# Performance work log

Hardware: AMD Instinct MI355X
Metric: run time of the kernel (lower is better)

Reference implementation:

```python
import jax, jax.numpy as jnp
import numpy as np

N = 12288          # atoms
G = 12             # graphs in batch
R = 1536           # residues
K = 32             # max_num_neighbors
RADIUS = 5.0
MIN_DISTANCE = 5
EPS = 1e-10


def setup_inputs() -> dict:
    key = jax.random.key(0)
    k1, k2, k3 = jax.random.split(key, 3)
    # positions in a 50 A box -> protein-like density (~a few neighbors in r=5)
    node_position = jax.random.uniform(k1, (N, 3), dtype=jnp.float32) * 50.0
    node2graph = jnp.sort(jax.random.randint(k2, (N,), 0, G, dtype=jnp.int32))
    atom2residue = jnp.sort(jax.random.randint(k3, (N,), 0, R, dtype=jnp.int32))
    return {"node_position": node_position, "node2graph": node2graph,
            "atom2residue": atom2residue}


def _select_neighbors(node_position, node2graph):
    """For each node i, pick up to K nearest same-graph nodes within RADIUS.
    Returns idx [N,K] (neighbor indices) and in_radius [N,K] (validity)."""
    n = node_position.shape[0]
    sq = jnp.sum(node_position * node_position, axis=-1)            # [N]
    d2 = sq[:, None] + sq[None, :] - 2.0 * (node_position @ node_position.T)
    d2 = jnp.maximum(d2, 0.0)                                        # [N,N]
    ar = jnp.arange(n)
    valid = (node2graph[:, None] == node2graph[None, :]) \
            & (ar[:, None] != ar[None, :]) \
            & (d2 <= RADIUS * RADIUS)
    nd2 = jnp.where(valid, d2, jnp.inf)
    neg_d2, idx = jax.lax.top_k(-nd2, K)                             # nearest K
    in_radius = jnp.isfinite(neg_d2)
    return idx, in_radius


def reference(node_position, node2graph, atom2residue):
    n = node_position.shape[0]
    idx, in_radius = _select_neighbors(node_position, node2graph)
    node_out = jnp.repeat(jnp.arange(n, dtype=jnp.int32), K)         # center i
    node_in = idx.reshape(-1).astype(jnp.int32)                      # neighbor j
    valid = in_radius.reshape(-1)
    # residue-distance filter: drop |res_in - res_out| < min_distance
    res_diff = jnp.abs(atom2residue[node_in] - atom2residue[node_out])
    valid = valid & (res_diff >= MIN_DISTANCE)
    # drop near-coincident positions (||p_i - p_j|| < eps)
    diff = node_position[node_in] - node_position[node_out]
    d2_sel = jnp.sum(diff * diff, axis=-1)
    valid = valid & (d2_sel >= EPS * EPS)
    relation = jnp.zeros_like(node_in)
    edge_list = jnp.stack([node_in, node_out, relation], axis=-1)    # [N*K,3]
    edge_list = jnp.where(valid[:, None], edge_list, -1)             # pad invalid
    return edge_list, valid, jnp.int32(1)
```

## Files before the change

### kernel.cpp

```cpp
#include <hip/hip_runtime.h>

#define EDGE_K 32
#define CAP    128
#define NB     64
#define DEPTH  8

__device__ __forceinline__ int prefix_count(unsigned long long mask) {
    return (int)__builtin_amdgcn_mbcnt_hi((unsigned)(mask >> 32),
                __builtin_amdgcn_mbcnt_lo((unsigned)mask, 0u));
}

__global__ __launch_bounds__(256) void pack_kernel(
    const float* __restrict__ pos, const int* __restrict__ n2g,
    float4* __restrict__ pk, int* __restrict__ bounds, int n)
{
    int i = blockIdx.x * blockDim.x + threadIdx.x;
    if (i >= n) return;
    pk[i] = make_float4(pos[3*i+0], pos[3*i+1], pos[3*i+2], 0.0f);
    const int gi = n2g[i];
    if (i == 0) {
        for (int g = 0; g <= gi && g < NB; ++g) bounds[g] = 0;
    } else {
        const int gp = n2g[i-1];
        if (gp != gi) for (int g = gp + 1; g <= gi && g < NB; ++g) bounds[g] = i;
    }
    if (i == n - 1) {
        for (int g = gi + 1; g < NB; ++g) bounds[g] = n;
    }
}

__global__ __launch_bounds__(64) void spatial_edge_fast(
    const float4* __restrict__ pk,
    const int* __restrict__ n2g,
    const int* __restrict__ a2r,
    const int* __restrict__ bounds,
    int* __restrict__ out, int n)
{
    const int i    = blockIdx.x;
    const int lane = threadIdx.x;

    __shared__ int2 scand[CAP];
    __shared__ int2 sres[EDGE_K];
    __shared__ int2 ebuf2[EDGE_K * 3 / 2];

    const float4 pi = pk[i];
    const float xi = pi.x, yi = pi.y, zi = pi.z;
    const float si = xi*xi + yi*yi + zi*zi;
    const int g  = n2g[i];
    const int ri = a2r[i];

    int jstart, jend;
    if (g < NB - 1) {
        jstart = bounds[g];
        jend   = bounds[g + 1];
    } else {
        int lo = 0, hi = n;
        while (lo < hi) { int m = (lo + hi) >> 1; if (n2g[m] < g) lo = m + 1; else hi = m; }
        jstart = lo; hi = n;
        while (lo < hi) { int m = (lo + hi) >> 1; if (n2g[m] <= g) lo = m + 1; else hi = m; }
        jend = lo;
    }

    int count = 0;
    auto process = [&](float4 p, int j) {
        bool pass = false; float d2 = 0.0f;
        if (j < jend && j != i) {
            const float sj2 = p.x*p.x + p.y*p.y + p.z*p.z;
            const float dt  = xi*p.x + yi*p.y + zi*p.z;
            d2 = si + sj2 - 2.0f*dt;
            d2 = fmaxf(d2, 0.0f);
            pass = (d2 <= 25.0f);
        }
        const unsigned long long mask = __ballot(pass);
        if (pass) {
            const int idx = count + prefix_count(mask);
            if (idx < CAP) scand[idx] = make_int2(__float_as_int(d2), j);
        }
        count += __popcll(mask);
    };

    const int nch  = (jend - jstart + 63) >> 6;
    const int jm   = jend - 1;
    const int base = jstart + lane;

    float4 buf[DEPTH];
#pragma unroll
    for (int u = 0; u < DEPTH; ++u)
        buf[u] = pk[min(base + (u << 6), jm)];

    for (int c = 0; c < nch; c += DEPTH) {
        float4 nxt[DEPTH];
        const int nb = base + ((c + DEPTH) << 6);
#pragma unroll
        for (int u = 0; u < DEPTH; ++u)
            nxt[u] = pk[min(nb + (u << 6), jm)];
        const int ja = jstart + (c << 6) + lane;
#pragma unroll
        for (int u = 0; u < DEPTH; ++u) {
            if (c + u < nch) process(buf[u], ja + (u << 6));
        }
#pragma unroll
        for (int u = 0; u < DEPTH; ++u) buf[u] = nxt[u];
    }
    __syncthreads();

    int cnt = 0;
    if (count <= CAP) {
        const int m = count;
        for (int c = lane; c < m; c += 64) {
            const int2 e = scand[c];
            const float dc = __int_as_float(e.x);
            int rank = 0;
            for (int t = 0; t < m; ++t) {
                const int2 et = scand[t];
                const float dtv = __int_as_float(et.x);
                rank += (dtv < dc) || (dtv == dc && et.y < e.y);
            }
            if (rank < EDGE_K) sres[rank] = e;
        }
        cnt = (m < EDGE_K) ? m : EDGE_K;
    } else {
        if (lane == 0) {
            float bd[EDGE_K]; int bj[EDGE_K]; int c2 = 0;
            for (int j = jstart; j < jend; ++j) {
                if (j == i) continue;
                const float4 p = pk[j];
                const float sj2 = p.x*p.x + p.y*p.y + p.z*p.z;
                const float dt  = xi*p.x + yi*p.y + zi*p.z;
                float d2 = si + sj2 - 2.0f*dt;
                d2 = fmaxf(d2, 0.0f);
                if (d2 > 25.0f) continue;
                if (c2 == EDGE_K && d2 >= bd[EDGE_K-1]) continue;
                int p2 = (c2 < EDGE_K) ? c2 : (EDGE_K - 1);
                while (p2 > 0 && bd[p2-1] > d2) { bd[p2] = bd[p2-1]; bj[p2] = bj[p2-1]; --p2; }
                bd[p2] = d2; bj[p2] = j;
                if (c2 < EDGE_K) ++c2;
            }
            for (int k = 0; k < c2; ++k) sres[k] = make_int2(__float_as_int(bd[k]), bj[k]);
        }
        cnt = (count < EDGE_K) ? count : EDGE_K;
    }
    __syncthreads();

    const int NK = n * EDGE_K;
    int* valid_out = out + 3 * NK;
    int* eb = (int*)ebuf2;
    if (lane < EDGE_K) {
        const int k = lane;
        int a = -1, b = -1, c = -1, v = 0;
        if (k < cnt) {
            const int j = sres[k].y;
            const int rj = a2r[j];
            const int rd = (rj > ri) ? (rj - ri) : (ri - rj);
            const float4 p = pk[j];
            const float dx = p.x - xi, dy = p.y - yi, dz = p.z - zi;
            const float d2s = dx*dx + dy*dy + dz*dz;
            if (rd >= 5 && d2s >= 1e-20f) { a = j; b = i; c = 0; v = 1; }
        }
        eb[3*k+0] = a;
        eb[3*k+1] = b;
        eb[3*k+2] = c;
        valid_out[i * EDGE_K + k] = v;
    }
    __syncthreads();
    if (lane < 48) {
        int2* eo = (int2*)(out + 3 * (i * EDGE_K));
        eo[lane] = ebuf2[lane];
    }
    if (i == 0 && lane == 0) out[4*NK] = 1;
}

__global__ __launch_bounds__(64) void spatial_edge_ref(
    const float* __restrict__ pos,
    const int* __restrict__ n2g,
    const int* __restrict__ a2r,
    int* __restrict__ out, int n)
{
    const int i = blockIdx.x;
    const int lane = threadIdx.x;
    __shared__ float sd2[CAP]; __shared__ int sj[CAP];
    __shared__ float rd2[EDGE_K]; __shared__ int rjj[EDGE_K];

    const float xi = pos[3*i+0], yi = pos[3*i+1], zi = pos[3*i+2];
    const float si = xi*xi + yi*yi + zi*zi;
    const int g = n2g[i]; const int ri = a2r[i];

    int lo = 0, hi = n;
    while (lo < hi) { int m = (lo + hi) >> 1; if (n2g[m] < g) lo = m + 1; else hi = m; }
    const int jstart = lo; hi = n;
    while (lo < hi) { int m = (lo + hi) >> 1; if (n2g[m] <= g) lo = m + 1; else hi = m; }
    const int jend = lo;

    int count = 0;
    for (int j0 = jstart; j0 < jend; j0 += 64) {
        const int j = j0 + lane;
        bool pass = false; float d2 = 0.0f;
        if (j < jend && j != i) {
            const float xj = pos[3*j+0], yj = pos[3*j+1], zj = pos[3*j+2];
            const float sj2 = xj*xj + yj*yj + zj*zj;
            const float dt  = xi*xj + yi*yj + zi*zj;
            d2 = fmaxf(si + sj2 - 2.0f*dt, 0.0f);
            pass = (d2 <= 25.0f);
        }
        const unsigned long long mask = __ballot(pass);
        if (pass) {
            const int idx = count + prefix_count(mask);
            if (idx < CAP) { sd2[idx] = d2; sj[idx] = j; }
        }
        count += __popcll(mask);
    }
    __syncthreads();

    int cnt;
    if (count <= CAP) {
        const int m = count;
        for (int c = lane; c < m; c += 64) {
            const float dc = sd2[c]; const int jc = sj[c];
            int rank = 0;
            for (int t = 0; t < m; ++t)
                rank += (sd2[t] < dc) || (sd2[t] == dc && sj[t] < jc);
            if (rank < EDGE_K) { rd2[rank] = dc; rjj[rank] = jc; }
        }
        cnt = (m < EDGE_K) ? m : EDGE_K;
    } else {
        if (lane == 0) {
            float bd[EDGE_K]; int bj[EDGE_K]; int c2 = 0;
            for (int j = jstart; j < jend; ++j) {
                if (j == i) continue;
                const float xj = pos[3*j+0], yj = pos[3*j+1], zj = pos[3*j+2];
                const float sj2 = xj*xj + yj*yj + zj*zj;
                const float dt  = xi*xj + yi*yj + zi*zj;
                float d2 = fmaxf(si + sj2 - 2.0f*dt, 0.0f);
                if (d2 > 25.0f) continue;
                if (c2 == EDGE_K && d2 >= bd[EDGE_K-1]) continue;
                int p = (c2 < EDGE_K) ? c2 : (EDGE_K - 1);
                while (p > 0 && bd[p-1] > d2) { bd[p] = bd[p-1]; bj[p] = bj[p-1]; --p; }
                bd[p] = d2; bj[p] = j;
                if (c2 < EDGE_K) ++c2;
            }
            for (int k = 0; k < c2; ++k) { rd2[k] = bd[k]; rjj[k] = bj[k]; }
        }
        cnt = (count < EDGE_K) ? count : EDGE_K;
    }
    __syncthreads();

    const int NK = n * EDGE_K;
    int* valid_out = out + 3 * NK;
    if (lane < EDGE_K) {
        const int k = lane;
        int a = -1, b = -1, c = -1, v = 0;
        if (k < cnt) {
            const int j = rjj[k];
            const int rj = a2r[j];
            const int rd = (rj > ri) ? (rj - ri) : (ri - rj);
            const float dx = pos[3*j+0] - xi, dy = pos[3*j+1] - yi, dz = pos[3*j+2] - zi;
            const float d2s = dx*dx + dy*dy + dz*dz;
            if (rd >= 5 && d2s >= 1e-20f) { a = j; b = i; c = 0; v = 1; }
        }
        const int e = i * EDGE_K + k;
        out[3*e+0] = a; out[3*e+1] = b; out[3*e+2] = c;
        valid_out[e] = v;
    }
    if (i == 0 && lane == 0) out[4*NK] = 1;
}

extern "C" void kernel_launch(void* const* d_in, const int* in_sizes, int n_in,
                              void* d_out, int out_size, void* d_ws, size_t ws_size,
                              hipStream_t stream) {
    const float* pos = (const float*)d_in[0];
    const int*   n2g = (const int*)d_in[1];
    const int*   a2r = (const int*)d_in[2];
    int* out = (int*)d_out;
    const int n = in_sizes[0] / 3;
    const size_t need = (size_t)n * sizeof(float4) + NB * sizeof(int);
    const bool packed = (ws_size >= need) && (((uintptr_t)d_ws & 15) == 0);
    if (packed) {
        float4* pk = (float4*)d_ws;
        int* bounds = (int*)(pk + n);
        hipLaunchKernelGGL(pack_kernel, dim3((n + 255) / 256), dim3(256), 0, stream,
                           pos, n2g, pk, bounds, n);
        hipLaunchKernelGGL(spatial_edge_fast, dim3(n), dim3(64), 0, stream,
                           (const float4*)pk, n2g, a2r, (const int*)bounds, out, n);
    } else {
        hipLaunchKernelGGL(spatial_edge_ref, dim3(n), dim3(64), 0, stream,
                           pos, n2g, a2r, out, n);
    }
}
```

Before: 29.23 us.

## Pack four independent wavefronts per block with per-wave shared buffers

Each block now runs four wavefronts, each handling its own atom with private slices of shared memory, so the grid shrinks fourfold. The block-wide barriers become block-scope memory fences on the assumption that one wave's lanes stay in lockstep. The goal is to cut per-block launch and scheduling overhead and raise occupancy for many tiny 64-thread blocks. It relies on intra-wave LDS ordering without a real barrier, which is fragile; an early return for out-of-range waves is safe only because no block barrier remains.

```diff
diff --git a/kernel.cpp b/kernel.cpp
--- a/kernel.cpp
+++ b/kernel.cpp
@@ -4,6 +4,7 @@
 #define CAP    128
 #define NB     64
 #define DEPTH  8
+#define WPB    4
 
 __device__ __forceinline__ int prefix_count(unsigned long long mask) {
     return (int)__builtin_amdgcn_mbcnt_hi((unsigned)(mask >> 32),
@@ -29,19 +30,21 @@
     }
 }
 
-__global__ __launch_bounds__(64) void spatial_edge_fast(
+__global__ __launch_bounds__(WPB * 64) void spatial_edge_fast(
     const float4* __restrict__ pk,
     const int* __restrict__ n2g,
     const int* __restrict__ a2r,
     const int* __restrict__ bounds,
     int* __restrict__ out, int n)
 {
-    const int i    = blockIdx.x;
-    const int lane = threadIdx.x;
-
-    __shared__ int2 scand[CAP];
-    __shared__ int2 sres[EDGE_K];
-    __shared__ int2 ebuf2[EDGE_K * 3 / 2];
+    const int wave = threadIdx.x >> 6;
+    const int lane = threadIdx.x & 63;
+    const int i    = blockIdx.x * WPB + wave;
+    if (i >= n) return;
+
+    __shared__ int2 scand[WPB][CAP];
+    __shared__ int2 sres[WPB][EDGE_K];
+    __shared__ int2 ebuf2[WPB][EDGE_K * 3 / 2];
 
     const float4 pi = pk[i];
     const float xi = pi.x, yi = pi.y, zi = pi.z;
@@ -74,7 +77,7 @@
         const unsigned long long mask = __ballot(pass);
         if (pass) {
             const int idx = count + prefix_count(mask);
-            if (idx < CAP) scand[idx] = make_int2(__float_as_int(d2), j);
+            if (idx < CAP) scand[wave][idx] = make_int2(__float_as_int(d2), j);
         }
         count += __popcll(mask);
     };
@@ -102,21 +105,21 @@
 #pragma unroll
         for (int u = 0; u < DEPTH; ++u) buf[u] = nxt[u];
     }
-    __syncthreads();
+    __threadfence_block();
 
     int cnt = 0;
     if (count <= CAP) {
         const int m = count;
         for (int c = lane; c < m; c += 64) {
-            const int2 e = scand[c];
+            const int2 e = scand[wave][c];
             const float dc = __int_as_float(e.x);
             int rank = 0;
             for (int t = 0; t < m; ++t) {
-                const int2 et = scand[t];
+                const int2 et = scand[wave][t];
                 const float dtv = __int_as_float(et.x);
                 rank += (dtv < dc) || (dtv == dc && et.y < e.y);
             }
-            if (rank < EDGE_K) sres[rank] = e;
+            if (rank < EDGE_K) sres[wave][rank] = e;
         }
         cnt = (m < EDGE_K) ? m : EDGE_K;
     } else {
@@ -136,20 +139,20 @@
                 bd[p2] = d2; bj[p2] = j;
                 if (c2 < EDGE_K) ++c2;
             }
-            for (int k = 0; k < c2; ++k) sres[k] = make_int2(__float_as_int(bd[k]), bj[k]);
+            for (int k = 0; k < c2; ++k) sres[wave][k] = make_int2(__float_as_int(bd[k]), bj[k]);
         }
         cnt = (count < EDGE_K) ? count : EDGE_K;
     }
-    __syncthreads();
+    __threadfence_block();
 
     const int NK = n * EDGE_K;
     int* valid_out = out + 3 * NK;
-    int* eb = (int*)ebuf2;
+    int* eb = (int*)&ebuf2[wave][0];
     if (lane < EDGE_K) {
         const int k = lane;
         int a = -1, b = -1, c = -1, v = 0;
         if (k < cnt) {
-            const int j = sres[k].y;
+            const int j = sres[wave][k].y;
             const int rj = a2r[j];
             const int rd = (rj > ri) ? (rj - ri) : (ri - rj);
             const float4 p = pk[j];
@@ -162,10 +165,10 @@
         eb[3*k+2] = c;
         valid_out[i * EDGE_K + k] = v;
     }
-    __syncthreads();
+    __threadfence_block();
     if (lane < 48) {
         int2* eo = (int2*)(out + 3 * (i * EDGE_K));
-        eo[lane] = ebuf2[lane];
+        eo[lane] = ebuf2[wave][lane];
     }
     if (i == 0 && lane == 0) out[4*NK] = 1;
 }
@@ -279,7 +282,8 @@
         int* bounds = (int*)(pk + n);
         hipLaunchKernelGGL(pack_kernel, dim3((n + 255) / 256), dim3(256), 0, stream,
                            pos, n2g, pk, bounds, n);
-        hipLaunchKernelGGL(spatial_edge_fast, dim3(n), dim3(64), 0, stream,
+        const int grid = (n + WPB - 1) / WPB;
+        hipLaunchKernelGGL(spatial_edge_fast, dim3(grid), dim3(WPB * 64), 0, stream,
                            (const float4*)pk, n2g, a2r, (const int*)bounds, out, n);
     } else {
         hipLaunchKernelGGL(spatial_edge_ref, dim3(n), dim3(64), 0, stream,
```

Measured after the change: 39.55 us. 35.3% more time.
